# Kernel optimization log

Hardware: AMD Instinct MI355X
Metric: run time of the kernel (lower is better)

The kernel has to match this reference:

```python
import jax, jax.numpy as jnp
import numpy as np

B, N, F_IN, S, F_OUT = 16, 128, 8, 8, 64
KN_HID = 32  # kernel_network=[32]
FC_HID = 32


def setup_inputs() -> dict:
    key = jax.random.key(0)
    ks = jax.random.split(key, 13)
    # sparse-ish binary adjacency (batch mode, dense storage)
    A = (jax.random.uniform(ks[0], (B, N, N)) < 0.1).astype(jnp.float32)
    X = jax.random.normal(ks[1], (B, N, F_IN), jnp.float32)
    E = jax.random.normal(ks[2], (B, N, N, S), jnp.float32)
    sc = 0.1
    return {
        "A": A, "X": X, "E": E,
        # ECCConv edge-kernel network: Dense(32, relu) -> Dense(F_IN*F_OUT, linear)
        "kn_w1": jax.random.normal(ks[3], (S, KN_HID), jnp.float32) * sc,
        "kn_b1": jnp.zeros((KN_HID,), jnp.float32),
        "kn_w2": jax.random.normal(ks[4], (KN_HID, F_IN * F_OUT), jnp.float32) * sc,
        "kn_b2": jnp.zeros((F_IN * F_OUT,), jnp.float32),
        # ECCConv root weight + bias
        "root_w": jax.random.normal(ks[5], (F_IN, F_OUT), jnp.float32) * sc,
        "conv_b": jnp.zeros((F_OUT,), jnp.float32),
        # Dense(32, relu)
        "fc_w": jax.random.normal(ks[6], (F_OUT, FC_HID), jnp.float32) * sc,
        "fc_b": jnp.zeros((FC_HID,), jnp.float32),
        # Dense(1, sigmoid)
        "out_w": jax.random.normal(ks[7], (FC_HID, 1), jnp.float32) * sc,
        "out_b": jnp.zeros((1,), jnp.float32),
    }


def reference(A, X, E, kn_w1, kn_b1, kn_w2, kn_b2, root_w, conv_b,
              fc_w, fc_b, out_w, out_b):
    # --- ECCConv (Spektral, batch mode) ---
    # edge-conditioned kernel network: per edge-pair MLP
    h = jax.nn.relu(E @ kn_w1 + kn_b1)            # [B,N,N,32]
    kernel = h @ kn_w2 + kn_b2                    # [B,N,N,F_in*F_out]
    kernel = kernel.reshape(A.shape[0], A.shape[1], A.shape[2], X.shape[-1], root_w.shape[-1])
    kernel = kernel * A[..., None, None]          # mask by adjacency
    # out[b,n,o] = sum_{i,f} kernel[b,n,i,f,o] * X[b,i,f]
    out = jnp.einsum("bnifo,bif->bno", kernel, X)
    out = out + X @ root_w + conv_b               # root weight + bias
    x = jax.nn.relu(out)                          # [B,N,F_out]
    # --- GlobalAvgPool over nodes ---
    x = x.mean(axis=1)                            # [B,F_out]
    # --- Dense head ---
    x = jax.nn.relu(x @ fc_w + fc_b)              # [B,32]
    return jax.nn.sigmoid(x @ out_w + out_b)      # [B,1]
```

## Files before the change

### kernel.cpp

```cpp
#include <hip/hip_runtime.h>
#include <math.h>

#define B_    16
#define N_    128
#define F_IN_ 8
#define S_    8
#define F_OUT_ 64
#define KN_HID_ 32
#define FC_HID_ 32

#define NODE_OFF  0

__device__ __forceinline__ int next_edge(unsigned long long& lo,
                                         unsigned long long& hi) {
    if (lo) { int i = __builtin_ctzll(lo); lo &= lo - 1; return i; }
    if (hi) { int i = __builtin_ctzll(hi) + 64; hi &= hi - 1; return i; }
    return -1;
}

__global__ __launch_bounds__(512) void k2_fused(
    const float* __restrict__ A, const float* __restrict__ X,
    const float* __restrict__ E,
    const float* __restrict__ kn_w1, const float* __restrict__ kn_b1,
    const float* __restrict__ kn_w2, const float* __restrict__ kn_b2,
    const float* __restrict__ root_w, const float* __restrict__ conv_b,
    float* __restrict__ ws)
{
    __shared__ float Xlds[N_ * F_IN_];
    __shared__ float Elds[8][N_ * S_];
    __shared__ float Tlds[8][264];
    __shared__ float Red[8][8][F_OUT_];
    __shared__ float Pool[8][F_OUT_];

    const int t    = threadIdx.x;
    const int lane = t & 63;
    const int wave = t >> 6;
    const int h2   = lane >> 5;
    const int j    = lane & 31;
    const int b    = blockIdx.x >> 4;
    const int bn   = blockIdx.x * 8 + wave;

    ((float2*)Xlds)[t] = ((const float2*)(X + b * N_ * F_IN_))[t];

    {
        const float4* __restrict__ src = (const float4*)(E + (size_t)bn * N_ * S_);
        float4* __restrict__ dst = (float4*)Elds[wave];
#pragma unroll
        for (int r = 0; r < 4; ++r)
            dst[lane + 64 * r] = src[lane + 64 * r];
    }

    float w1j[S_];
#pragma unroll
    for (int s = 0; s < S_; ++s) w1j[s] = kn_w1[s * KN_HID_ + j];
    const float b1j = kn_b1[j];

    const float a0 = A[(size_t)bn * N_ + lane];
    const float a1 = A[(size_t)bn * N_ + 64 + lane];
    unsigned long long mlo = __ballot(a0 != 0.f);
    unsigned long long mhi = __ballot(a1 != 0.f);

    __syncthreads();

    const float4* __restrict__ Xl4 = (const float4*)Xlds;
    const float4* __restrict__ El4 = (const float4*)Elds[wave];

    float T[4]  = {0.f, 0.f, 0.f, 0.f};
    float xs[4] = {0.f, 0.f, 0.f, 0.f};

    int i0 = next_edge(mlo, mhi);
    float4 eA0, eA1;
    if (i0 >= 0) { eA0 = El4[i0 * 2]; eA1 = El4[i0 * 2 + 1]; }
    int i1 = (i0 >= 0) ? next_edge(mlo, mhi) : -1;
    float4 eB0, eB1;
    if (i1 >= 0) { eB0 = El4[i1 * 2]; eB1 = El4[i1 * 2 + 1]; }

    while (i0 >= 0) {
        const int i2 = (i1 >= 0) ? next_edge(mlo, mhi) : -1;
        float4 eC0, eC1;
        if (i2 >= 0) { eC0 = El4[i2 * 2]; eC1 = El4[i2 * 2 + 1]; }

        const float ha = fmaf(eA0.x, w1j[0], fmaf(eA0.y, w1j[1],
                         fmaf(eA0.z, w1j[2], eA0.w * w1j[3])));
        const float hb = fmaf(eA1.x, w1j[4], fmaf(eA1.y, w1j[5],
                         fmaf(eA1.z, w1j[6], eA1.w * w1j[7])));
        float hv = b1j + ha + hb;
        hv = hv > 0.f ? hv : 0.f;

        const float4 xf = Xl4[i0 * 2 + h2];
        T[0] = fmaf(hv, xf.x, T[0]);  T[1] = fmaf(hv, xf.y, T[1]);
        T[2] = fmaf(hv, xf.z, T[2]);  T[3] = fmaf(hv, xf.w, T[3]);
        xs[0] += xf.x; xs[1] += xf.y; xs[2] += xf.z; xs[3] += xf.w;

        i0 = i1; eA0 = eB0; eA1 = eB1;
        i1 = i2; eB0 = eC0; eB1 = eC1;
    }

    float4* __restrict__ Tl4 = (float4*)Tlds[wave];
    Tl4[j * 2 + h2] = make_float4(T[0], T[1], T[2], T[3]);
    if (j == 0)
        Tl4[64 + h2] = make_float4(xs[0], xs[1], xs[2], xs[3]);

    __syncthreads();

    const int q = lane & 15;
    const int g = lane >> 4;
    const float4* __restrict__ W4 = (const float4*)kn_w2;
    const float4* __restrict__ B4 = (const float4*)kn_b2;
    const int base = wave * 32;

    float4 acc[8];
#pragma unroll
    for (int nd = 0; nd < 8; ++nd) acc[nd] = make_float4(0.f, 0.f, 0.f, 0.f);

#pragma unroll
    for (int kf2 = g; kf2 < 32; kf2 += 4) {
        const int kf = base + kf2;
        const float4 w = W4[kf * 16 + q];
#pragma unroll
        for (int nd = 0; nd < 8; ++nd) {
            const float tv = Tlds[nd][kf];
            acc[nd].x = fmaf(tv, w.x, acc[nd].x);
            acc[nd].y = fmaf(tv, w.y, acc[nd].y);
            acc[nd].z = fmaf(tv, w.z, acc[nd].z);
            acc[nd].w = fmaf(tv, w.w, acc[nd].w);
        }
    }
    if (g == 0) {
        const float4 w = B4[wave * 16 + q];
#pragma unroll
        for (int nd = 0; nd < 8; ++nd) {
            const float tv = Tlds[nd][256 + wave];
            acc[nd].x = fmaf(tv, w.x, acc[nd].x);
            acc[nd].y = fmaf(tv, w.y, acc[nd].y);
            acc[nd].z = fmaf(tv, w.z, acc[nd].z);
            acc[nd].w = fmaf(tv, w.w, acc[nd].w);
        }
    }

#pragma unroll
    for (int d = 16; d < 64; d <<= 1) {
#pragma unroll
        for (int nd = 0; nd < 8; ++nd) {
            acc[nd].x += __shfl_xor(acc[nd].x, d);
            acc[nd].y += __shfl_xor(acc[nd].y, d);
            acc[nd].z += __shfl_xor(acc[nd].z, d);
            acc[nd].w += __shfl_xor(acc[nd].w, d);
        }
    }

    if (g == 0) {
#pragma unroll
        for (int nd = 0; nd < 8; ++nd)
            ((float4*)Red[wave][nd])[q] = acc[nd];
    }
    __syncthreads();

    if (g == 0) {
        const float4 cb = ((const float4*)conv_b)[q];
        float4 r = cb;
#pragma unroll
        for (int pw = 0; pw < 8; ++pw) {
            const float4 p = ((const float4*)Red[pw][wave])[q];
            r.x += p.x; r.y += p.y; r.z += p.z; r.w += p.w;
        }
        const int n = bn & (N_ - 1);
        const float4* __restrict__ R4 = (const float4*)root_w;
#pragma unroll
        for (int f = 0; f < F_IN_; ++f) {
            const float xv = Xlds[n * F_IN_ + f];
            const float4 rw = R4[f * 16 + q];
            r.x = fmaf(xv, rw.x, r.x); r.y = fmaf(xv, rw.y, r.y);
            r.z = fmaf(xv, rw.z, r.z); r.w = fmaf(xv, rw.w, r.w);
        }
        r.x = r.x > 0.f ? r.x : 0.f;  r.y = r.y > 0.f ? r.y : 0.f;
        r.z = r.z > 0.f ? r.z : 0.f;  r.w = r.w > 0.f ? r.w : 0.f;
        ((float4*)Pool[wave])[q] = r;
    }
    __syncthreads();

    if (wave == 0) {
        float s = 0.f;
#pragma unroll
        for (int nd = 0; nd < 8; ++nd) s += Pool[nd][lane];
        ws[NODE_OFF + (size_t)blockIdx.x * F_OUT_ + lane] = s;
    }
}

__global__ __launch_bounds__(256) void k3_head(
    const float* __restrict__ fc_w, const float* __restrict__ fc_b,
    const float* __restrict__ out_w, const float* __restrict__ out_b,
    const float* __restrict__ ws, float* __restrict__ out)
{
    const int b = blockIdx.x;
    const int t = threadIdx.x;
    const int o = t & 63;
    const int g = t >> 6;

    float p = 0.f;
    for (int s = g; s < 16; s += 4)
        p += ws[NODE_OFF + (size_t)(b * 16 + s) * F_OUT_ + o];

    __shared__ float red[4][F_OUT_];
    __shared__ float pm[F_OUT_];
    __shared__ float y[FC_HID_];
    red[g][o] = p;
    __syncthreads();

    if (t < F_OUT_)
        pm[t] = (red[0][t] + red[1][t] + red[2][t] + red[3][t]) * (1.0f / (float)N_);
    __syncthreads();

    if (t < FC_HID_) {
        float v = fc_b[t];
#pragma unroll
        for (int o2 = 0; o2 < F_OUT_; ++o2) v += pm[o2] * fc_w[o2 * FC_HID_ + t];
        y[t] = v > 0.f ? v : 0.f;
    }
    __syncthreads();

    if (t == 0) {
        float z = out_b[0];
#pragma unroll
        for (int qq = 0; qq < FC_HID_; ++qq) z += y[qq] * out_w[qq];
        out[b] = 1.f / (1.f + expf(-z));
    }
}

extern "C" void kernel_launch(void* const* d_in, const int* in_sizes, int n_in,
                              void* d_out, int out_size, void* d_ws, size_t ws_size,
                              hipStream_t stream)
{
    const float* A      = (const float*)d_in[0];
    const float* X      = (const float*)d_in[1];
    const float* E      = (const float*)d_in[2];
    const float* kn_w1  = (const float*)d_in[3];
    const float* kn_b1  = (const float*)d_in[4];
    const float* kn_w2  = (const float*)d_in[5];
    const float* kn_b2  = (const float*)d_in[6];
    const float* root_w = (const float*)d_in[7];
    const float* conv_b = (const float*)d_in[8];
    const float* fc_w   = (const float*)d_in[9];
    const float* fc_b   = (const float*)d_in[10];
    const float* out_w  = (const float*)d_in[11];
    const float* out_b  = (const float*)d_in[12];

    float* ws  = (float*)d_ws;
    float* out = (float*)d_out;

    k2_fused<<<B_ * N_ / 8, 512, 0, stream>>>(A, X, E, kn_w1, kn_b1,
                                              kn_w2, kn_b2, root_w, conv_b, ws);
    k3_head<<<B_, 256, 0, stream>>>(fc_w, fc_b, out_w, out_b, ws, out);
}
```

Measured before the change: 96.08 us.

## Gather only adjacent-edge E rows instead of staging full E row in LDS

Instead of copying each node's full 128x8 edge-feature row into LDS, each wave enumerates the adjacency bitmask and gathers only the E entries for existing edges (up to 40) into a packed LDS buffer. A fallback path for denser rows reads E directly from global memory and broadcasts features with shuffles. This cuts global traffic on E by roughly the adjacency density, which is the dominant memory cost. The kn_w2 and kn_b2 loads are also hoisted into registers before the barrier so their latency overlaps the edge loop, at the cost of more registers and a serial bitmask scan per lane.

```diff
diff --git a/kernel.cpp b/kernel.cpp
--- a/kernel.cpp
+++ b/kernel.cpp
@@ -10,6 +10,8 @@
 #define FC_HID_ 32
 
 #define NODE_OFF  0
+
+#define MAX_GATHER 40
 
 __device__ __forceinline__ int next_edge(unsigned long long& lo,
                                          unsigned long long& hi) {
@@ -27,7 +29,7 @@
     float* __restrict__ ws)
 {
     __shared__ float Xlds[N_ * F_IN_];
-    __shared__ float Elds[8][N_ * S_];
+    __shared__ float Epack[8][MAX_GATHER * S_];
     __shared__ float Tlds[8][264];
     __shared__ float Red[8][8][F_OUT_];
     __shared__ float Pool[8][F_OUT_];
@@ -39,16 +41,10 @@
     const int j    = lane & 31;
     const int b    = blockIdx.x >> 4;
     const int bn   = blockIdx.x * 8 + wave;
+    const int sub  = lane & 7;
+    const int eg   = lane >> 3;
 
     ((float2*)Xlds)[t] = ((const float2*)(X + b * N_ * F_IN_))[t];
-
-    {
-        const float4* __restrict__ src = (const float4*)(E + (size_t)bn * N_ * S_);
-        float4* __restrict__ dst = (float4*)Elds[wave];
-#pragma unroll
-        for (int r = 0; r < 4; ++r)
-            dst[lane + 64 * r] = src[lane + 64 * r];
-    }
 
     float w1j[S_];
 #pragma unroll
@@ -60,41 +56,112 @@
     unsigned long long mlo = __ballot(a0 != 0.f);
     unsigned long long mhi = __ballot(a1 != 0.f);
 
+    int e0 = -1, e1 = -1, e2 = -1, e3 = -1, e4 = -1;
+    int cnt;
+    {
+        unsigned long long glo = mlo, ghi = mhi;
+        int s = 0;
+        while (true) {
+            const int i = next_edge(glo, ghi);
+            if (i < 0) break;
+            if ((s & 7) == eg) {
+                const int r = s >> 3;
+                if      (r == 0) e0 = i;
+                else if (r == 1) e1 = i;
+                else if (r == 2) e2 = i;
+                else if (r == 3) e3 = i;
+                else if (r == 4) e4 = i;
+            }
+            ++s;
+        }
+        cnt = s;
+    }
+
+    const float* __restrict__ Erow = E + (size_t)bn * (N_ * S_);
+    const bool gather = (cnt <= MAX_GATHER);
+    if (gather) {
+        float* __restrict__ Ep = Epack[wave];
+        if (e0 >= 0) Ep[(      eg) * 8 + sub] = Erow[e0 * 8 + sub];
+        if (e1 >= 0) Ep[( 8  + eg) * 8 + sub] = Erow[e1 * 8 + sub];
+        if (e2 >= 0) Ep[(16  + eg) * 8 + sub] = Erow[e2 * 8 + sub];
+        if (e3 >= 0) Ep[(24  + eg) * 8 + sub] = Erow[e3 * 8 + sub];
+        if (e4 >= 0) Ep[(32  + eg) * 8 + sub] = Erow[e4 * 8 + sub];
+    }
+
     __syncthreads();
 
     const float4* __restrict__ Xl4 = (const float4*)Xlds;
-    const float4* __restrict__ El4 = (const float4*)Elds[wave];
 
     float T[4]  = {0.f, 0.f, 0.f, 0.f};
     float xs[4] = {0.f, 0.f, 0.f, 0.f};
 
-    int i0 = next_edge(mlo, mhi);
-    float4 eA0, eA1;
-    if (i0 >= 0) { eA0 = El4[i0 * 2]; eA1 = El4[i0 * 2 + 1]; }
-    int i1 = (i0 >= 0) ? next_edge(mlo, mhi) : -1;
-    float4 eB0, eB1;
-    if (i1 >= 0) { eB0 = El4[i1 * 2]; eB1 = El4[i1 * 2 + 1]; }
-
-    while (i0 >= 0) {
-        const int i2 = (i1 >= 0) ? next_edge(mlo, mhi) : -1;
-        float4 eC0, eC1;
-        if (i2 >= 0) { eC0 = El4[i2 * 2]; eC1 = El4[i2 * 2 + 1]; }
-
-        const float ha = fmaf(eA0.x, w1j[0], fmaf(eA0.y, w1j[1],
-                         fmaf(eA0.z, w1j[2], eA0.w * w1j[3])));
-        const float hb = fmaf(eA1.x, w1j[4], fmaf(eA1.y, w1j[5],
-                         fmaf(eA1.z, w1j[6], eA1.w * w1j[7])));
-        float hv = b1j + ha + hb;
-        hv = hv > 0.f ? hv : 0.f;
-
-        const float4 xf = Xl4[i0 * 2 + h2];
-        T[0] = fmaf(hv, xf.x, T[0]);  T[1] = fmaf(hv, xf.y, T[1]);
-        T[2] = fmaf(hv, xf.z, T[2]);  T[3] = fmaf(hv, xf.w, T[3]);
-        xs[0] += xf.x; xs[1] += xf.y; xs[2] += xf.z; xs[3] += xf.w;
-
-        i0 = i1; eA0 = eB0; eA1 = eB1;
-        i1 = i2; eB0 = eC0; eB1 = eC1;
-    }
+    if (gather) {
+        const float4* __restrict__ Ep4 = (const float4*)Epack[wave];
+        int i0 = next_edge(mlo, mhi);
+        float4 eA0, eA1;
+        if (i0 >= 0) { eA0 = Ep4[0]; eA1 = Ep4[1]; }
+        int i1 = (i0 >= 0) ? next_edge(mlo, mhi) : -1;
+        float4 eB0, eB1;
+        if (i1 >= 0) { eB0 = Ep4[2]; eB1 = Ep4[3]; }
+        int nslot = 2;
+
+        while (i0 >= 0) {
+            const int i2 = (i1 >= 0) ? next_edge(mlo, mhi) : -1;
+            float4 eC0, eC1;
+            if (i2 >= 0) { eC0 = Ep4[nslot * 2]; eC1 = Ep4[nslot * 2 + 1]; ++nslot; }
+
+            const float ha = fmaf(eA0.x, w1j[0], fmaf(eA0.y, w1j[1],
+                             fmaf(eA0.z, w1j[2], eA0.w * w1j[3])));
+            const float hb = fmaf(eA1.x, w1j[4], fmaf(eA1.y, w1j[5],
+                             fmaf(eA1.z, w1j[6], eA1.w * w1j[7])));
+            float hv = b1j + ha + hb;
+            hv = hv > 0.f ? hv : 0.f;
+
+            const float4 xf = Xl4[i0 * 2 + h2];
+            T[0] = fmaf(hv, xf.x, T[0]);  T[1] = fmaf(hv, xf.y, T[1]);
+            T[2] = fmaf(hv, xf.z, T[2]);  T[3] = fmaf(hv, xf.w, T[3]);
+            xs[0] += xf.x; xs[1] += xf.y; xs[2] += xf.z; xs[3] += xf.w;
+
+            i0 = i1; eA0 = eB0; eA1 = eB1;
+            i1 = i2; eB0 = eC0; eB1 = eC1;
+        }
+    } else {
+        const float* __restrict__ Eb = Erow + sub;
+        int i0 = next_edge(mlo, mhi);
+        float p0 = (i0 >= 0) ? Eb[i0 * S_] : 0.f;
+        int i1 = (i0 >= 0) ? next_edge(mlo, mhi) : -1;
+        float p1 = (i1 >= 0) ? Eb[i1 * S_] : 0.f;
+
+        while (i0 >= 0) {
+            const int i2 = (i1 >= 0) ? next_edge(mlo, mhi) : -1;
+            const float p2 = (i2 >= 0) ? Eb[i2 * S_] : 0.f;
+
+            const float ha = fmaf(__shfl(p0, 0), w1j[0], fmaf(__shfl(p0, 1), w1j[1],
+                             fmaf(__shfl(p0, 2), w1j[2], __shfl(p0, 3) * w1j[3])));
+            const float hb = fmaf(__shfl(p0, 4), w1j[4], fmaf(__shfl(p0, 5), w1j[5],
+                             fmaf(__shfl(p0, 6), w1j[6], __shfl(p0, 7) * w1j[7])));
+            float hv = b1j + ha + hb;
+            hv = hv > 0.f ? hv : 0.f;
+
+            const float4 xf = Xl4[i0 * 2 + h2];
+            T[0] = fmaf(hv, xf.x, T[0]);  T[1] = fmaf(hv, xf.y, T[1]);
+            T[2] = fmaf(hv, xf.z, T[2]);  T[3] = fmaf(hv, xf.w, T[3]);
+            xs[0] += xf.x; xs[1] += xf.y; xs[2] += xf.z; xs[3] += xf.w;
+
+            i0 = i1; p0 = p1;
+            i1 = i2; p1 = p2;
+        }
+    }
+
+    const int q = lane & 15;
+    const int g = lane >> 4;
+    const float4* __restrict__ W4 = (const float4*)kn_w2;
+    const int base = wave * 32;
+    float4 wreg[8];
+#pragma unroll
+    for (int r = 0; r < 8; ++r)
+        wreg[r] = W4[(base + r * 4 + g) * 16 + q];
+    const float4 wb = ((const float4*)kn_b2)[wave * 16 + q];
 
     float4* __restrict__ Tl4 = (float4*)Tlds[wave];
     Tl4[j * 2 + h2] = make_float4(T[0], T[1], T[2], T[3]);
@@ -103,20 +170,14 @@
 
     __syncthreads();
 
-    const int q = lane & 15;
-    const int g = lane >> 4;
-    const float4* __restrict__ W4 = (const float4*)kn_w2;
-    const float4* __restrict__ B4 = (const float4*)kn_b2;
-    const int base = wave * 32;
-
     float4 acc[8];
 #pragma unroll
     for (int nd = 0; nd < 8; ++nd) acc[nd] = make_float4(0.f, 0.f, 0.f, 0.f);
 
 #pragma unroll
-    for (int kf2 = g; kf2 < 32; kf2 += 4) {
-        const int kf = base + kf2;
-        const float4 w = W4[kf * 16 + q];
+    for (int r = 0; r < 8; ++r) {
+        const int kf = base + r * 4 + g;
+        const float4 w = wreg[r];
 #pragma unroll
         for (int nd = 0; nd < 8; ++nd) {
             const float tv = Tlds[nd][kf];
@@ -127,14 +188,13 @@
         }
     }
     if (g == 0) {
-        const float4 w = B4[wave * 16 + q];
 #pragma unroll
         for (int nd = 0; nd < 8; ++nd) {
             const float tv = Tlds[nd][256 + wave];
-            acc[nd].x = fmaf(tv, w.x, acc[nd].x);
-            acc[nd].y = fmaf(tv, w.y, acc[nd].y);
-            acc[nd].z = fmaf(tv, w.z, acc[nd].z);
-            acc[nd].w = fmaf(tv, w.w, acc[nd].w);
+            acc[nd].x = fmaf(tv, wb.x, acc[nd].x);
+            acc[nd].y = fmaf(tv, wb.y, acc[nd].y);
+            acc[nd].z = fmaf(tv, wb.z, acc[nd].z);
+            acc[nd].w = fmaf(tv, wb.w, acc[nd].w);
         }
     }
 
```

After: 97.16 us. No clear change (+1.1%).
